# Kernel optimization log

Hardware: AMD Instinct MI355X
Metric: run time of the kernel (lower is better)

## Reference

```python
import jax, jax.numpy as jnp
import numpy as np

D_MODEL = 1024
NUM_HEADS = 16
D_K = D_MODEL // NUM_HEADS
B, S = 4, 2048


def setup_inputs() -> dict:
    key = jax.random.key(0)
    k1, k2, k3 = jax.random.split(key, 3)
    x = jax.random.normal(k1, (B, S, D_MODEL), dtype=jnp.float32)
    w_qkv = jax.random.normal(k2, (3, NUM_HEADS, D_K, D_MODEL), dtype=jnp.float32) / np.sqrt(D_MODEL)
    w_o = jax.random.normal(k3, (D_MODEL, D_MODEL), dtype=jnp.float32) / np.sqrt(D_MODEL)
    return {"x": x, "w_qkv": w_qkv, "w_o": w_o}


def reference(x, w_qkv, w_o):
    # x: [b, s, m]; w_qkv: [3, h, k, m]; w_o: [m, m]
    seq_len = x.shape[-2]
    d_k = w_qkv.shape[-2]
    # fused QKV projection for all heads: [3, b, h, s, k]
    qkv = jnp.einsum('bsm,qhkm->qbhsk', x, w_qkv)
    Q, K, V = qkv[0], qkv[1], qkv[2]
    # attention scores [b, h, s, s]
    scores = jnp.einsum('bhsk,bhtk->bhst', Q, K) / jnp.sqrt(jnp.asarray(d_k, x.dtype))
    # causal mask: position t > s is masked
    causal = jnp.tril(jnp.ones((seq_len, seq_len), dtype=bool))
    scores = jnp.where(causal, scores, -jnp.inf)
    probs = jax.nn.softmax(scores, axis=-1)
    # attn_pdrop = 0.0 -> dropout is identity
    attn = jnp.einsum('bhst,bhtk->bhsk', probs, V)
    # concat heads: [b, s, h*k]
    b, h, s, k = attn.shape
    attn_cat = jnp.transpose(attn, (0, 2, 1, 3)).reshape(b, s, h * k)
    # output projection: y = attn_cat @ w_o^T
    return jnp.einsum('bsd,md->bsm', attn_cat, w_o)
```

## Files before the change

kernel.cpp:

```cpp
#include <hip/hip_runtime.h>
#include <hip/hip_bf16.h>


#define D_MODEL 1024
#define NUM_HEADS 16
#define D_KD 64
#define B_SZ 4
#define S_LEN 2048
#define ROWS (B_SZ * S_LEN)
#define QKV_N (3 * D_MODEL)

typedef __attribute__((ext_vector_type(8))) short short8;
typedef __attribute__((ext_vector_type(4))) float f32x4;
typedef __attribute__((ext_vector_type(16))) float f32x16;
typedef unsigned short ushort_t;

__device__ __forceinline__ unsigned f2bf(float f) {
    unsigned u = __builtin_bit_cast(unsigned, f);
    return (u + 0x7FFFu + ((u >> 16) & 1u)) >> 16;
}
__device__ __forceinline__ uint2 pack_bf16x4(float4 v) {
    uint2 u;
    u.x = f2bf(v.x) | (f2bf(v.y) << 16);
    u.y = f2bf(v.z) | (f2bf(v.w) << 16);
    return u;
}
__device__ __forceinline__ void gload16(void* lds, const void* g) {
    __builtin_amdgcn_global_load_lds(
        (const __attribute__((address_space(1))) unsigned int*)(g),
        (__attribute__((address_space(3))) unsigned int*)(lds), 16, 0, 0);
}

__global__ __launch_bounds__(256) void cvt_bf16(const float* __restrict__ src,
                                                ushort_t* __restrict__ dst, int n4) {
    int i = blockIdx.x * blockDim.x + threadIdx.x;
    const int stride = gridDim.x * blockDim.x;
    for (; i < n4; i += stride) {
        float4 v = reinterpret_cast<const float4*>(src)[i];
        *reinterpret_cast<uint2*>(&dst[(size_t)i * 4]) = pack_bf16x4(v);
    }
}

template <int MODE>
__global__ __launch_bounds__(256) void gemm_bt_bf16(const ushort_t* __restrict__ A,
                                                    const ushort_t* __restrict__ Bm,
                                                    ushort_t* __restrict__ Cb,
                                                    float* __restrict__ Cf,
                                                    int M, int N, int K) {
    __shared__ ushort_t As[128 * 32];
    __shared__ ushort_t Bs[128 * 32];

    const int t = threadIdx.x;
    const int lane = t & 63;
    const int w = t >> 6;
    const int wr = w >> 1, wc = w & 1;
    const int row0 = blockIdx.y * 128;
    const int col0 = blockIdx.x * 128;

    const int srow = t >> 2;
    const int sk8 = (t & 3) << 3;

    const ushort_t* Ag = A + (size_t)(row0 + srow) * K + sk8;
    const ushort_t* Bg = Bm + (size_t)(col0 + srow) * K + sk8;
    ushort_t* ldsA0 = &As[(size_t)t * 8];
    ushort_t* ldsA1 = &As[(size_t)(t + 256) * 8];
    ushort_t* ldsB0 = &Bs[(size_t)t * 8];
    ushort_t* ldsB1 = &Bs[(size_t)(t + 256) * 8];

    f32x4 acc[4][4];
#pragma unroll
    for (int m = 0; m < 4; ++m)
#pragma unroll
        for (int n = 0; n < 4; ++n)
#pragma unroll
            for (int j = 0; j < 4; ++j) acc[m][n][j] = 0.f;

    const int q8 = (lane >> 4) << 3;
    const int frA = wr * 64 + (lane & 15);
    const int frB = wc * 64 + (lane & 15);
    const int NT = K >> 5;

    for (int kt = 0; kt < NT; ++kt) {
        const int k0 = kt << 5;
        __syncthreads();
        gload16(ldsA0, Ag + k0);
        gload16(ldsA1, Ag + (size_t)64 * K + k0);
        gload16(ldsB0, Bg + k0);
        gload16(ldsB1, Bg + (size_t)64 * K + k0);
        __syncthreads();

        short8 afr[4], bfr[4];
#pragma unroll
        for (int m = 0; m < 4; ++m)
            afr[m] = *reinterpret_cast<const short8*>(&As[(frA + m * 16) * 32 + q8]);
#pragma unroll
        for (int n = 0; n < 4; ++n)
            bfr[n] = *reinterpret_cast<const short8*>(&Bs[(frB + n * 16) * 32 + q8]);
#pragma unroll
        for (int m = 0; m < 4; ++m)
#pragma unroll
            for (int n = 0; n < 4; ++n)
                acc[m][n] = __builtin_amdgcn_mfma_f32_16x16x32_bf16(afr[m], bfr[n],
                                                                    acc[m][n], 0, 0, 0);
    }

    const int orow = row0 + wr * 64 + ((lane >> 4) << 2);
    const int ocol = col0 + wc * 64 + (lane & 15);
#pragma unroll
    for (int m = 0; m < 4; ++m)
#pragma unroll
        for (int n = 0; n < 4; ++n) {
            const int cg = ocol + n * 16;
#pragma unroll
            for (int j = 0; j < 4; ++j) {
                const int rg = orow + m * 16 + j;
                float v = acc[m][n][j];
                if (MODE == 0) {
                    const int q = cg >> 10, hh = (cg >> 6) & 15, kk = cg & 63;
                    const int bb = rg >> 11, s = rg & 2047;
                    if (q == 0) v *= 0.125f;
                    Cb[((((size_t)q * B_SZ + bb) * NUM_HEADS + hh) * S_LEN + s) * D_KD + kk] =
                        (ushort_t)f2bf(v);
                } else {
                    Cf[(size_t)rg * N + cg] = v;
                }
            }
        }
}

__global__ __launch_bounds__(512, 2) void flash_attn_mfma_v3(const ushort_t* __restrict__ qkv,
                                                             ushort_t* __restrict__ attn_out) {
    const int qb = (int)gridDim.x - 1 - (int)blockIdx.x;
    const int h = blockIdx.y;
    const int b = blockIdx.z;
    const int t = threadIdx.x;
    const int lane = t & 63;
    const int w = t >> 6;
    const int l31 = lane & 31;
    const int hi = lane >> 5;

    __shared__ ushort_t smem[256 * 72];
    __shared__ float fbuf[8][32];
    ushort_t* Qs = smem;
    ushort_t* Ks = smem;
    ushort_t* Vt = smem + 64 * 72;

    const size_t head_elems = (size_t)S_LEN * D_KD;
    const ushort_t* Qg = qkv + (((size_t)0 * B_SZ + b) * NUM_HEADS + h) * head_elems;
    const ushort_t* Kg = qkv + (((size_t)1 * B_SZ + b) * NUM_HEADS + h) * head_elems;
    const ushort_t* Vg = qkv + (((size_t)2 * B_SZ + b) * NUM_HEADS + h) * head_elems;

    const int q0 = qb * 256;
    const int qmin = q0 + 32 * w;

#pragma unroll
    for (int lx = 0; lx < 4; ++lx) {
        int idx = t + lx * 512;
        int r = idx >> 3;
        int c8 = (idx & 7) << 3;
        *reinterpret_cast<uint4*>(&Qs[r * 72 + c8]) =
            *reinterpret_cast<const uint4*>(&Qg[(size_t)(q0 + r) * D_KD + c8]);
    }
    __syncthreads();

    short8 qfr[4];
#pragma unroll
    for (int ks = 0; ks < 4; ++ks)
        qfr[ks] = *reinterpret_cast<const short8*>(&Qs[(32 * w + l31) * 72 + 16 * ks + 8 * hi]);

    f32x16 oacc[2];
#pragma unroll
    for (int n = 0; n < 2; ++n)
#pragma unroll
        for (int j = 0; j < 16; ++j) oacc[n][j] = 0.f;
    float m = -1e30f, lsum = 0.f;

    const int nt = 4 * (qb + 1);
    for (int tt = 0; tt < nt; ++tt) {
        const int c0 = tt * 64;
        __syncthreads();

        if (w < 4) {
#pragma unroll
            for (int i = 0; i < 2; ++i) {
                int j = t + i * 256;
                int r = j >> 3;
                int c8 = (j & 7) << 3;
                *reinterpret_cast<uint4*>(&Ks[r * 72 + c8]) =
                    *reinterpret_cast<const uint4*>(&Kg[(size_t)(c0 + r) * D_KD + c8]);
            }
        } else {
            int t2 = t - 256;
            int tp = t2 & 31, dg = t2 >> 5;
            int t0 = tp * 2, d0 = dg * 8;
            uint4 va = *reinterpret_cast<const uint4*>(&Vg[(size_t)(c0 + t0) * D_KD + d0]);
            uint4 vb = *reinterpret_cast<const uint4*>(&Vg[(size_t)(c0 + t0 + 1) * D_KD + d0]);
            const ushort_t* ua = reinterpret_cast<const ushort_t*>(&va);
            const ushort_t* ub = reinterpret_cast<const ushort_t*>(&vb);
#pragma unroll
            for (int d = 0; d < 8; ++d) {
                unsigned u = (unsigned)ua[d] | ((unsigned)ub[d] << 16);
                *reinterpret_cast<unsigned*>(&Vt[(d0 + d) * 72 + t0]) = u;
            }
        }
        __syncthreads();

        for (int st = 0; st < 2; ++st) {
            const int t0s = c0 + 32 * st;
            if (t0s > qmin) break;
            const bool diag = (t0s == qmin);

            f32x16 s;
#pragma unroll
            for (int j = 0; j < 16; ++j) s[j] = 0.f;
            __builtin_amdgcn_s_setprio(1);
#pragma unroll
            for (int ks = 0; ks < 4; ++ks) {
                short8 ka = *reinterpret_cast<const short8*>(
                    &Ks[(32 * st + l31) * 72 + 16 * ks + 8 * hi]);
                s = __builtin_amdgcn_mfma_f32_32x32x16_bf16(ka, qfr[ks], s, 0, 0, 0);
            }
            __builtin_amdgcn_s_setprio(0);
            if (diag) {
#pragma unroll
                for (int reg = 0; reg < 16; ++reg) {
                    const int tloc = (reg & 3) + 8 * (reg >> 2) + 4 * hi;
                    if (tloc > l31) s[reg] = -1e30f;
                }
            }

            float pm = s[0];
#pragma unroll
            for (int reg = 1; reg < 16; ++reg) pm = fmaxf(pm, s[reg]);
            pm = fmaxf(pm, __shfl_xor(pm, 32));

            if (!__all(pm <= m + 8.0f)) {
                const float mnew = fmaxf(m, pm);
                const float al = __expf(m - mnew);
                m = mnew;
                lsum *= al;
                fbuf[w][l31] = al;
#pragma unroll
                for (int g = 0; g < 4; ++g) {
                    float4 a4 = *reinterpret_cast<float4*>(&fbuf[w][8 * g + 4 * hi]);
                    const float* ap = reinterpret_cast<const float*>(&a4);
#pragma unroll
                    for (int j = 0; j < 4; ++j) {
                        oacc[0][4 * g + j] *= ap[j];
                        oacc[1][4 * g + j] *= ap[j];
                    }
                }
            }

            float p[16];
            float ps = 0.f;
#pragma unroll
            for (int reg = 0; reg < 16; ++reg) {
                p[reg] = __expf(s[reg] - m);
                ps += p[reg];
            }
            ps += __shfl_xor(ps, 32);
            lsum += ps;

            unsigned pk[8], sw[8];
#pragma unroll
            for (int i = 0; i < 8; ++i) pk[i] = f2bf(p[2 * i]) | (f2bf(p[2 * i + 1]) << 16);
#pragma unroll
            for (int i = 0; i < 8; ++i) sw[i] = (unsigned)__shfl_xor((int)pk[i], 32);

            union { unsigned u[4]; short8 s8; } a0, a1;
            a0.u[0] = hi ? sw[2] : pk[0];
            a0.u[1] = hi ? sw[3] : pk[1];
            a0.u[2] = hi ? pk[2] : sw[0];
            a0.u[3] = hi ? pk[3] : sw[1];
            a1.u[0] = hi ? sw[6] : pk[4];
            a1.u[1] = hi ? sw[7] : pk[5];
            a1.u[2] = hi ? pk[6] : sw[4];
            a1.u[3] = hi ? pk[7] : sw[5];

            __builtin_amdgcn_s_setprio(1);
#pragma unroll
            for (int n = 0; n < 2; ++n) {
                const ushort_t* vrow = &Vt[(32 * n + l31) * 72 + 32 * st + 8 * hi];
                short8 vb0 = *reinterpret_cast<const short8*>(vrow);
                short8 vb1 = *reinterpret_cast<const short8*>(vrow + 16);
                oacc[n] = __builtin_amdgcn_mfma_f32_32x32x16_bf16(a0.s8, vb0, oacc[n], 0, 0, 0);
                oacc[n] = __builtin_amdgcn_mfma_f32_32x32x16_bf16(a1.s8, vb1, oacc[n], 0, 0, 0);
            }
            __builtin_amdgcn_s_setprio(0);
        }
    }

    const float inv = 1.f / lsum;
    fbuf[w][l31] = inv;
#pragma unroll
    for (int g = 0; g < 4; ++g) {
        float4 i4 = *reinterpret_cast<float4*>(&fbuf[w][8 * g + 4 * hi]);
        const float* ip = reinterpret_cast<const float*>(&i4);
#pragma unroll
        for (int j = 0; j < 4; ++j) {
            const int reg = 4 * g + j;
            const int qrow = q0 + 32 * w + 8 * g + 4 * hi + j;
            const size_t base = ((size_t)(b * S_LEN + qrow)) * D_MODEL + h * D_KD + l31;
            attn_out[base] = (ushort_t)f2bf(oacc[0][reg] * ip[j]);
            attn_out[base + 32] = (ushort_t)f2bf(oacc[1][reg] * ip[j]);
        }
    }
}

extern "C" void kernel_launch(void* const* d_in, const int* in_sizes, int n_in,
                              void* d_out, int out_size, void* d_ws, size_t ws_size,
                              hipStream_t stream) {
    const float* x = (const float*)d_in[0];
    const float* w_qkv = (const float*)d_in[1];
    const float* w_o = (const float*)d_in[2];
    float* out = (float*)d_out;

    ushort_t* xb = (ushort_t*)d_ws;
    ushort_t* wqb = xb + 8388608;
    ushort_t* wob = wqb + 3145728;
    ushort_t* qkvb = wob + 1048576;
    ushort_t* attnb = qkvb + 25165824;

    cvt_bf16<<<2048, 256, 0, stream>>>(x, xb, 8388608 / 4);
    cvt_bf16<<<1024, 256, 0, stream>>>(w_qkv, wqb, 3145728 / 4);
    cvt_bf16<<<512, 256, 0, stream>>>(w_o, wob, 1048576 / 4);

    gemm_bt_bf16<0><<<dim3(QKV_N / 128, ROWS / 128), dim3(256), 0, stream>>>(
        xb, wqb, qkvb, nullptr, ROWS, QKV_N, D_MODEL);
    flash_attn_mfma_v3<<<dim3(S_LEN / 256, NUM_HEADS, B_SZ), dim3(512), 0, stream>>>(qkvb, attnb);
    gemm_bt_bf16<1><<<dim3(D_MODEL / 128, ROWS / 128), dim3(256), 0, stream>>>(
        attnb, wob, nullptr, out, ROWS, D_MODEL, D_MODEL);
}
```

Before: 311.7 us.

## Prefetch next K/V tile into registers and switch softmax to exp2 domain

The flash attention kernel now loads the next K/V tile from global memory into registers right after the LDS barrier, so the global latency overlaps with the MFMA work on the current tile. The softmax runs in base 2: Q is pre-scaled by log2(e)/8, exp is replaced with exp2f, and the lazy-rescale threshold is scaled to match. The manual bf16 rounding is also replaced with the intrinsic __float2bfloat16. Holding the prefetched tile costs extra registers, which may hurt occupancy under the launch bound of 512 threads with 2 blocks.

```diff
diff --git a/kernel.cpp b/kernel.cpp
--- a/kernel.cpp
+++ b/kernel.cpp
@@ -10,20 +10,19 @@
 #define ROWS (B_SZ * S_LEN)
 #define QKV_N (3 * D_MODEL)
 
+#define QSCALE 0.18033688f
+#define DEFER_THR 11.5415603f
+
 typedef __attribute__((ext_vector_type(8))) short short8;
 typedef __attribute__((ext_vector_type(4))) float f32x4;
 typedef __attribute__((ext_vector_type(16))) float f32x16;
 typedef unsigned short ushort_t;
 
-__device__ __forceinline__ unsigned f2bf(float f) {
-    unsigned u = __builtin_bit_cast(unsigned, f);
-    return (u + 0x7FFFu + ((u >> 16) & 1u)) >> 16;
-}
-__device__ __forceinline__ uint2 pack_bf16x4(float4 v) {
-    uint2 u;
-    u.x = f2bf(v.x) | (f2bf(v.y) << 16);
-    u.y = f2bf(v.z) | (f2bf(v.w) << 16);
-    return u;
+__device__ __forceinline__ ushort_t bf1(float a) {
+    return __builtin_bit_cast(unsigned short, __float2bfloat16(a));
+}
+__device__ __forceinline__ unsigned packbf2(float a, float b) {
+    return (unsigned)bf1(a) | ((unsigned)bf1(b) << 16);
 }
 __device__ __forceinline__ void gload16(void* lds, const void* g) {
     __builtin_amdgcn_global_load_lds(
@@ -37,7 +36,10 @@
     const int stride = gridDim.x * blockDim.x;
     for (; i < n4; i += stride) {
         float4 v = reinterpret_cast<const float4*>(src)[i];
-        *reinterpret_cast<uint2*>(&dst[(size_t)i * 4]) = pack_bf16x4(v);
+        uint2 u;
+        u.x = packbf2(v.x, v.y);
+        u.y = packbf2(v.z, v.w);
+        *reinterpret_cast<uint2*>(&dst[(size_t)i * 4]) = u;
     }
 }
 
@@ -118,9 +120,9 @@
                 if (MODE == 0) {
                     const int q = cg >> 10, hh = (cg >> 6) & 15, kk = cg & 63;
                     const int bb = rg >> 11, s = rg & 2047;
-                    if (q == 0) v *= 0.125f;
+                    if (q == 0) v *= QSCALE;
                     Cb[((((size_t)q * B_SZ + bb) * NUM_HEADS + hh) * S_LEN + s) * D_KD + kk] =
-                        (ushort_t)f2bf(v);
+                        bf1(v);
                 } else {
                     Cf[(size_t)rg * N + cg] = v;
                 }
@@ -128,7 +130,7 @@
         }
 }
 
-__global__ __launch_bounds__(512, 2) void flash_attn_mfma_v3(const ushort_t* __restrict__ qkv,
+__global__ __launch_bounds__(512, 2) void flash_attn_mfma_v4(const ushort_t* __restrict__ qkv,
                                                              ushort_t* __restrict__ attn_out) {
     const int qb = (int)gridDim.x - 1 - (int)blockIdx.x;
     const int h = blockIdx.y;
@@ -152,6 +154,19 @@
 
     const int q0 = qb * 256;
     const int qmin = q0 + 32 * w;
+    const int nt = 4 * (qb + 1);
+
+    const int krow0 = t >> 3, kc8 = (t & 7) << 3;
+    const int tp = (t & 31) * 2, dg8 = ((t & 255) >> 5) << 3;
+
+    uint4 kreg0, kreg1, vreg0, vreg1;
+    if (w < 4) {
+        kreg0 = *reinterpret_cast<const uint4*>(&Kg[(size_t)krow0 * D_KD + kc8]);
+        kreg1 = *reinterpret_cast<const uint4*>(&Kg[(size_t)(krow0 + 32) * D_KD + kc8]);
+    } else {
+        vreg0 = *reinterpret_cast<const uint4*>(&Vg[(size_t)tp * D_KD + dg8]);
+        vreg1 = *reinterpret_cast<const uint4*>(&Vg[(size_t)(tp + 1) * D_KD + dg8]);
+    }
 
 #pragma unroll
     for (int lx = 0; lx < 4; ++lx) {
@@ -175,36 +190,35 @@
         for (int j = 0; j < 16; ++j) oacc[n][j] = 0.f;
     float m = -1e30f, lsum = 0.f;
 
-    const int nt = 4 * (qb + 1);
     for (int tt = 0; tt < nt; ++tt) {
-        const int c0 = tt * 64;
         __syncthreads();
 
         if (w < 4) {
-#pragma unroll
-            for (int i = 0; i < 2; ++i) {
-                int j = t + i * 256;
-                int r = j >> 3;
-                int c8 = (j & 7) << 3;
-                *reinterpret_cast<uint4*>(&Ks[r * 72 + c8]) =
-                    *reinterpret_cast<const uint4*>(&Kg[(size_t)(c0 + r) * D_KD + c8]);
-            }
+            *reinterpret_cast<uint4*>(&Ks[krow0 * 72 + kc8]) = kreg0;
+            *reinterpret_cast<uint4*>(&Ks[(krow0 + 32) * 72 + kc8]) = kreg1;
         } else {
-            int t2 = t - 256;
-            int tp = t2 & 31, dg = t2 >> 5;
-            int t0 = tp * 2, d0 = dg * 8;
-            uint4 va = *reinterpret_cast<const uint4*>(&Vg[(size_t)(c0 + t0) * D_KD + d0]);
-            uint4 vb = *reinterpret_cast<const uint4*>(&Vg[(size_t)(c0 + t0 + 1) * D_KD + d0]);
-            const ushort_t* ua = reinterpret_cast<const ushort_t*>(&va);
-            const ushort_t* ub = reinterpret_cast<const ushort_t*>(&vb);
+            const ushort_t* ua = reinterpret_cast<const ushort_t*>(&vreg0);
+            const ushort_t* ub = reinterpret_cast<const ushort_t*>(&vreg1);
 #pragma unroll
             for (int d = 0; d < 8; ++d) {
                 unsigned u = (unsigned)ua[d] | ((unsigned)ub[d] << 16);
-                *reinterpret_cast<unsigned*>(&Vt[(d0 + d) * 72 + t0]) = u;
+                *reinterpret_cast<unsigned*>(&Vt[(dg8 + d) * 72 + tp]) = u;
             }
         }
         __syncthreads();
 
+        if (tt + 1 < nt) {
+            const int cn = (tt + 1) * 64;
+            if (w < 4) {
+                kreg0 = *reinterpret_cast<const uint4*>(&Kg[(size_t)(cn + krow0) * D_KD + kc8]);
+                kreg1 = *reinterpret_cast<const uint4*>(&Kg[(size_t)(cn + krow0 + 32) * D_KD + kc8]);
+            } else {
+                vreg0 = *reinterpret_cast<const uint4*>(&Vg[(size_t)(cn + tp) * D_KD + dg8]);
+                vreg1 = *reinterpret_cast<const uint4*>(&Vg[(size_t)(cn + tp + 1) * D_KD + dg8]);
+            }
+        }
+
+        const int c0 = tt * 64;
         for (int st = 0; st < 2; ++st) {
             const int t0s = c0 + 32 * st;
             if (t0s > qmin) break;
@@ -234,9 +248,9 @@
             for (int reg = 1; reg < 16; ++reg) pm = fmaxf(pm, s[reg]);
             pm = fmaxf(pm, __shfl_xor(pm, 32));
 
-            if (!__all(pm <= m + 8.0f)) {
+            if (!__all(pm <= m + DEFER_THR)) {
                 const float mnew = fmaxf(m, pm);
-                const float al = __expf(m - mnew);
+                const float al = exp2f(m - mnew);
                 m = mnew;
                 lsum *= al;
                 fbuf[w][l31] = al;
@@ -256,7 +270,7 @@
             float ps = 0.f;
 #pragma unroll
             for (int reg = 0; reg < 16; ++reg) {
-                p[reg] = __expf(s[reg] - m);
+                p[reg] = exp2f(s[reg] - m);
                 ps += p[reg];
             }
             ps += __shfl_xor(ps, 32);
@@ -264,7 +278,7 @@
 
             unsigned pk[8], sw[8];
 #pragma unroll
-            for (int i = 0; i < 8; ++i) pk[i] = f2bf(p[2 * i]) | (f2bf(p[2 * i + 1]) << 16);
+            for (int i = 0; i < 8; ++i) pk[i] = packbf2(p[2 * i], p[2 * i + 1]);
 #pragma unroll
             for (int i = 0; i < 8; ++i) sw[i] = (unsigned)__shfl_xor((int)pk[i], 32);
 
@@ -302,8 +316,8 @@
             const int reg = 4 * g + j;
             const int qrow = q0 + 32 * w + 8 * g + 4 * hi + j;
             const size_t base = ((size_t)(b * S_LEN + qrow)) * D_MODEL + h * D_KD + l31;
-            attn_out[base] = (ushort_t)f2bf(oacc[0][reg] * ip[j]);
-            attn_out[base + 32] = (ushort_t)f2bf(oacc[1][reg] * ip[j]);
+            attn_out[base] = bf1(oacc[0][reg] * ip[j]);
+            attn_out[base + 32] = bf1(oacc[1][reg] * ip[j]);
         }
     }
 }
@@ -328,7 +342,7 @@
 
     gemm_bt_bf16<0><<<dim3(QKV_N / 128, ROWS / 128), dim3(256), 0, stream>>>(
         xb, wqb, qkvb, nullptr, ROWS, QKV_N, D_MODEL);
-    flash_attn_mfma_v3<<<dim3(S_LEN / 256, NUM_HEADS, B_SZ), dim3(512), 0, stream>>>(qkvb, attnb);
+    flash_attn_mfma_v4<<<dim3(S_LEN / 256, NUM_HEADS, B_SZ), dim3(512), 0, stream>>>(qkvb, attnb);
     gemm_bt_bf16<1><<<dim3(D_MODEL / 128, ROWS / 128), dim3(256), 0, stream>>>(
         attnb, wob, nullptr, out, ROWS, D_MODEL, D_MODEL);
 }
```

Measured after the change: 310.2 us. About the same (-0.5%).
